# Performance work log

Measured on AMD Instinct MI355X. Metric: run time of the kernel, lower is better.

## Reference

```python
import jax, jax.numpy as jnp
import numpy as np

N_EXAMPLES = 10  # hardcoded repeat_interleave(10) in the source

def setup_inputs() -> dict:
    key = jax.random.key(0)
    k1, k2, k3, k4 = jax.random.split(key, 4)
    B, L, S, H = 8, 256, 512, 1024
    return {
        "output": jax.random.normal(k1, (B * N_EXAMPLES, L, H), dtype=jnp.float32),
        "context0": jax.random.normal(k2, (B * N_EXAMPLES, L, H), dtype=jnp.float32),
        "context1": jax.random.normal(k3, (B, S, H), dtype=jnp.float32),
        "mask": jnp.zeros((B * N_EXAMPLES, L), dtype=bool),
        "W_out": jax.random.normal(k4, (H, 3 * H), dtype=jnp.float32) * 0.02,
        "b_out": jnp.zeros((H,), dtype=jnp.float32),
    }

def reference(output, context0, context1, mask, W_out, b_out):
    # output, context0: [B*10, L, H]; context1: [B, S, H]
    # NOTE: in the torch source, `attn.data.masked_fill(mask, -inf)` is NOT
    # in-place and its result is discarded, so the mask has no effect on the
    # math. We reproduce that faithfully: `mask` is unused.
    del mask
    set_ctx = jnp.repeat(context1, N_EXAMPLES, axis=0)  # [B*10, S, H]
    # example-attention branch: bmm -> softmax -> bmm
    ex_attn = jax.nn.softmax(jnp.einsum('bld,bsd->bls', output, context0), axis=-1)  # [B*10, L, L]
    # set-attention branch: bmm -> softmax -> bmm
    set_attn = jax.nn.softmax(jnp.einsum('bld,bsd->bls', output, set_ctx), axis=-1)  # [B*10, L, S]
    ex_c = jnp.einsum('bls,bsd->bld', ex_attn, context0)   # [B*10, L, H]
    set_c = jnp.einsum('bls,bsd->bld', set_attn, set_ctx)  # [B*10, L, H]
    all_info = jnp.concatenate([output, ex_c, set_c], axis=-1)  # [B*10, L, 3H]
    out = jnp.tanh(jnp.einsum('blk,hk->blh', all_info, W_out) + b_out)  # [B*10, L, H]
    return (out, ex_attn, set_attn)
```

## Files before the change

### kernel.cpp

```cpp
#include <hip/hip_runtime.h>
#include <stdint.h>
#include <math.h>

typedef unsigned short u16;
typedef __attribute__((ext_vector_type(8))) short short8;
typedef __attribute__((ext_vector_type(4))) float floatx4;

__device__ __forceinline__ u16 f32_to_bf16(float f) {
    union { float f; uint32_t u; } v; v.f = f;
    uint32_t r = v.u + 0x7FFF + ((v.u >> 16) & 1);
    return (u16)(r >> 16);
}
__device__ __forceinline__ float bf16_to_f32(u16 h) {
    union { uint32_t u; float f; } v; v.u = ((uint32_t)h) << 16; return v.f;
}

__device__ __forceinline__ void gl_lds16(const u16* g, u16* l) {
    __builtin_amdgcn_global_load_lds(
        (const __attribute__((address_space(1))) void*)g,
        (__attribute__((address_space(3))) void*)l, 16, 0, 0);
}


__global__ void split_kernel(const float4* __restrict__ x, ushort4* __restrict__ hi,
                             ushort4* __restrict__ lo, long n4) {
    long i = (long)blockIdx.x * blockDim.x + threadIdx.x;
    if (i >= n4) return;
    float4 v = x[i];
    ushort4 h, l;
    h.x = f32_to_bf16(v.x); l.x = f32_to_bf16(v.x - bf16_to_f32(h.x));
    h.y = f32_to_bf16(v.y); l.y = f32_to_bf16(v.y - bf16_to_f32(h.y));
    h.z = f32_to_bf16(v.z); l.z = f32_to_bf16(v.z - bf16_to_f32(h.z));
    h.w = f32_to_bf16(v.w); l.w = f32_to_bf16(v.w - bf16_to_f32(h.w));
    hi[i] = h; lo[i] = l;
}

__global__ void conv_kernel(const float4* __restrict__ x, ushort4* __restrict__ hi, long n4) {
    long i = (long)blockIdx.x * blockDim.x + threadIdx.x;
    if (i >= n4) return;
    float4 v = x[i];
    ushort4 h;
    h.x = f32_to_bf16(v.x); h.y = f32_to_bf16(v.y);
    h.z = f32_to_bf16(v.z); h.w = f32_to_bf16(v.w);
    hi[i] = h;
}

__global__ void transpose_u16(const u16* __restrict__ src, u16* __restrict__ dst,
                              int R, int C) {
    __shared__ u16 tile[32][34];
    long base = (long)blockIdx.z * R * C;
    int c0 = blockIdx.x * 32, r0 = blockIdx.y * 32;
    #pragma unroll
    for (int i = threadIdx.y; i < 32; i += 8)
        tile[i][threadIdx.x] = src[base + (long)(r0 + i) * C + c0 + threadIdx.x];
    __syncthreads();
    #pragma unroll
    for (int i = threadIdx.y; i < 32; i += 8)
        dst[base + (long)(c0 + i) * R + r0 + threadIdx.x] = tile[threadIdx.x][i];
}

template <int VPT>
__global__ void softmax_rows(float* __restrict__ data, u16* __restrict__ outb) {
    int row = blockIdx.x * 4 + (threadIdx.x >> 6);
    int lane = threadIdx.x & 63;
    long base = (long)row * (VPT * 64) + lane;
    float v[VPT];
    #pragma unroll
    for (int i = 0; i < VPT; ++i) v[i] = data[base + i * 64];
    float m = v[0];
    #pragma unroll
    for (int i = 1; i < VPT; ++i) m = fmaxf(m, v[i]);
    #pragma unroll
    for (int off = 32; off > 0; off >>= 1) m = fmaxf(m, __shfl_xor(m, off, 64));
    float s = 0.f;
    #pragma unroll
    for (int i = 0; i < VPT; ++i) { v[i] = __expf(v[i] - m); s += v[i]; }
    #pragma unroll
    for (int off = 32; off > 0; off >>= 1) s += __shfl_xor(s, off, 64);
    float inv = 1.0f / s;
    #pragma unroll
    for (int i = 0; i < VPT; ++i) {
        float r = v[i] * inv;
        data[base + i * 64] = r;
        outb[base + i * 64] = f32_to_bf16(r);
    }
}

struct GemmP {
    const u16* A[3];
    const u16* B[3];
    const u16* B2[3];
    long strideAb, strideBb, strideB2b, strideCb, strideC2b;
    int bdiv, bdiv2, nseg, Kper, lda, ldb, ldb2, ldc, ldc2, mode;
    int gx, gy, nx1;
    float* Cf; float* Cf2; u16* Cb; const float* bias;
};

__global__ __launch_bounds__(256) void gemm_bt(GemmP p) {
    __shared__ u16 As[128 * 64];
    __shared__ u16 Bs[128 * 64];
    const int tid  = threadIdx.x;
    const int lane = tid & 63;
    const int wave = tid >> 6;
    const int quad = lane >> 4;
    const int l15  = lane & 15;
    const int wm = (wave & 1) * 64;
    const int wn = (wave >> 1) * 64;

    const int f  = blockIdx.x;
    const int Tx = gridDim.x >> 3;
    const int t  = (f & 7) * Tx + (f >> 3);
    const int n  = t % p.gx;
    const int r  = t / p.gx;
    const int m0 = (r % p.gy) * 128;
    const int bz = r / p.gy;

    const u16* Bsegs[3];
    int ldb, ldc, nn, bdv;
    long bstr, cstr;
    float* Cf;
    if (n < p.nx1) {
        Bsegs[0] = p.B[0]; Bsegs[1] = p.B[1]; Bsegs[2] = p.B[2];
        ldb = p.ldb; ldc = p.ldc; bstr = p.strideBb; cstr = p.strideCb;
        Cf = p.Cf; bdv = p.bdiv; nn = n;
    } else {
        Bsegs[0] = p.B2[0]; Bsegs[1] = p.B2[1]; Bsegs[2] = p.B2[2];
        ldb = p.ldb2; ldc = p.ldc2; bstr = p.strideB2b; cstr = p.strideC2b;
        Cf = p.Cf2; bdv = p.bdiv2; nn = n - p.nx1;
    }
    const int n0 = nn * 128;

    const int stg_r8 = tid >> 3;
    const int stg_c  = ((tid & 7) ^ (stg_r8 & 7)) * 8;
    const int xorl   = l15 & 7;

    floatx4 acc[4][4];
    #pragma unroll
    for (int i = 0; i < 4; ++i)
        #pragma unroll
        for (int j = 0; j < 4; ++j)
            acc[i][j] = (floatx4){0.f, 0.f, 0.f, 0.f};

    const long aoff = (long)bz * p.strideAb + (long)m0 * p.lda;
    const long boff = (long)(bz / bdv) * bstr + (long)n0 * ldb;

    for (int seg = 0; seg < p.nseg; ++seg) {
        const u16* Ag = p.A[seg] + aoff;
        const u16* Bg = Bsegs[seg] + boff;
        for (int k0 = 0; k0 < p.Kper; k0 += 64) {
            __syncthreads();
            #pragma unroll
            for (int i = 0; i < 4; ++i) {
                const int rr = i * 32 + stg_r8;
                gl_lds16(Ag + (long)rr * p.lda + k0 + stg_c, &As[(i * 256 + tid) * 8]);
            }
            #pragma unroll
            for (int i = 0; i < 4; ++i) {
                const int rr = i * 32 + stg_r8;
                gl_lds16(Bg + (long)rr * ldb + k0 + stg_c, &Bs[(i * 256 + tid) * 8]);
            }
            __syncthreads();
            #pragma unroll
            for (int kk = 0; kk < 2; ++kk) {
                const int cs = ((kk * 4 + quad) ^ xorl) * 8;
                short8 af[4], bfr[4];
                #pragma unroll
                for (int i = 0; i < 4; ++i)
                    af[i] = *(const short8*)&As[(wm + i * 16 + l15) * 64 + cs];
                #pragma unroll
                for (int i = 0; i < 4; ++i)
                    bfr[i] = *(const short8*)&Bs[(wn + i * 16 + l15) * 64 + cs];
                #pragma unroll
                for (int mi = 0; mi < 4; ++mi)
                    #pragma unroll
                    for (int ni = 0; ni < 4; ++ni)
                        acc[mi][ni] = __builtin_amdgcn_mfma_f32_16x16x32_bf16(
                            af[mi], bfr[ni], acc[mi][ni], 0, 0, 0);
            }
        }
    }

    const long coff = (long)bz * cstr;
    const int rb = m0 + wm + quad * 4;
    const int cbase = n0 + wn + l15;
    if (p.mode == 2) {
        #pragma unroll
        for (int ni = 0; ni < 4; ++ni) {
            const float bv = p.bias[cbase + ni * 16];
            #pragma unroll
            for (int mi = 0; mi < 4; ++mi)
                #pragma unroll
                for (int j = 0; j < 4; ++j)
                    Cf[coff + (long)(rb + mi * 16 + j) * ldc + cbase + ni * 16] =
                        tanhf(acc[mi][ni][j] + bv);
        }
    } else if (p.mode == 0) {
        #pragma unroll
        for (int ni = 0; ni < 4; ++ni)
            #pragma unroll
            for (int mi = 0; mi < 4; ++mi)
                #pragma unroll
                for (int j = 0; j < 4; ++j)
                    Cf[coff + (long)(rb + mi * 16 + j) * ldc + cbase + ni * 16] =
                        acc[mi][ni][j];
    } else {
        #pragma unroll
        for (int ni = 0; ni < 4; ++ni)
            #pragma unroll
            for (int mi = 0; mi < 4; ++mi)
                #pragma unroll
                for (int j = 0; j < 4; ++j)
                    p.Cb[coff + (long)(rb + mi * 16 + j) * ldc + cbase + ni * 16] =
                        f32_to_bf16(acc[mi][ni][j]);
    }
}

extern "C" void kernel_launch(void* const* d_in, const int* in_sizes, int n_in,
                              void* d_out, int out_size, void* d_ws, size_t ws_size,
                              hipStream_t stream) {
    const int BT = 80, L = 256, S = 512, H = 1024;
    const long NO    = (long)BT * L * H;
    const long NC1   = (long)8 * S * H;
    const long NW    = (long)H * 3 * H;
    const long NEXA  = (long)BT * L * L;
    const long NSETA = (long)BT * L * S;

    const float* X    = (const float*)d_in[0];
    const float* C0   = (const float*)d_in[1];
    const float* C1   = (const float*)d_in[2];
    const float* Wf   = (const float*)d_in[4];
    const float* bias = (const float*)d_in[5];

    float* out  = (float*)d_out;
    float* exa  = out + NO;
    float* seta = exa + NEXA;

    char* wsb = (char*)d_ws;
    size_t off = 0;
    auto alloc = [&](long nbytes) -> void* {
        void* p = (void*)(wsb + off);
        off += ((size_t)nbytes + 255) & ~(size_t)255;
        return p;
    };
    u16* Xhi  = (u16*)alloc(NO * 2);
    u16* Xlo  = (u16*)alloc(NO * 2);
    u16* C0hi = (u16*)alloc(NO * 2);
    u16* C0lo = (u16*)alloc(NO * 2);
    u16* C1hi = (u16*)alloc(NC1 * 2);
    u16* C1lo = (u16*)alloc(NC1 * 2);
    u16* Wb   = (u16*)alloc(NW * 2);
    u16* exab = (u16*)alloc(NEXA * 2);
    u16* setab= (u16*)alloc(NSETA * 2);
    u16* C0T = C0lo;
    u16* C1T = C1lo;
    u16* exc = Xlo;
    u16* setc = C0hi;

    split_kernel<<<(int)(NO / 4 / 256), 256, 0, stream>>>((const float4*)X, (ushort4*)Xhi, (ushort4*)Xlo, NO / 4);
    split_kernel<<<(int)(NO / 4 / 256), 256, 0, stream>>>((const float4*)C0, (ushort4*)C0hi, (ushort4*)C0lo, NO / 4);
    split_kernel<<<(int)(NC1 / 4 / 256), 256, 0, stream>>>((const float4*)C1, (ushort4*)C1hi, (ushort4*)C1lo, NC1 / 4);
    conv_kernel<<<(int)(NW / 4 / 256), 256, 0, stream>>>((const float4*)Wf, (ushort4*)Wb, NW / 4);

    {
        GemmP p{};
        p.A[0] = Xhi;  p.A[1] = Xlo;  p.A[2] = Xhi;
        p.B[0]  = C0hi; p.B[1]  = C0hi; p.B[2]  = C0lo;
        p.B2[0] = C1hi; p.B2[1] = C1hi; p.B2[2] = C1lo;
        p.strideAb = (long)L * H;
        p.strideBb = (long)L * H;  p.strideB2b = (long)S * H;
        p.strideCb = (long)L * L;  p.strideC2b = (long)L * S;
        p.bdiv = 1; p.bdiv2 = 10;
        p.nseg = 3; p.Kper = H; p.lda = H; p.ldb = H; p.ldb2 = H;
        p.ldc = L; p.ldc2 = S; p.mode = 0;
        p.gx = 6; p.gy = 2; p.nx1 = 2;
        p.Cf = exa; p.Cf2 = seta;
        gemm_bt<<<dim3(6 * 2 * BT, 1, 1), 256, 0, stream>>>(p);
    }
    softmax_rows<4><<<BT * L / 4, 256, 0, stream>>>(exa, exab);
    softmax_rows<8><<<BT * L / 4, 256, 0, stream>>>(seta, setab);

    transpose_u16<<<dim3(H / 32, L / 32, BT), dim3(32, 8), 0, stream>>>(C0hi, C0T, L, H);
    transpose_u16<<<dim3(H / 32, S / 32, 8), dim3(32, 8), 0, stream>>>(C1hi, C1T, S, H);

    {
        GemmP p{};
        p.A[0] = exab; p.B[0] = C0T;
        p.strideAb = (long)L * L; p.strideBb = (long)H * L; p.strideCb = (long)L * H;
        p.bdiv = 1; p.nseg = 1; p.Kper = L; p.lda = L; p.ldb = L; p.ldc = H; p.mode = 1;
        p.gx = 8; p.gy = 2; p.nx1 = 8;
        p.Cb = exc;
        gemm_bt<<<dim3(8 * 2 * BT, 1, 1), 256, 0, stream>>>(p);
    }
    {
        GemmP p{};
        p.A[0] = setab; p.B[0] = C1T;
        p.strideAb = (long)L * S; p.strideBb = (long)H * S; p.strideCb = (long)L * H;
        p.bdiv = 10; p.nseg = 1; p.Kper = S; p.lda = S; p.ldb = S; p.ldc = H; p.mode = 1;
        p.gx = 8; p.gy = 2; p.nx1 = 8;
        p.Cb = setc;
        gemm_bt<<<dim3(8 * 2 * BT, 1, 1), 256, 0, stream>>>(p);
    }
    {
        GemmP p{};
        p.A[0] = Xhi; p.A[1] = exc; p.A[2] = setc;
        p.B[0] = Wb;  p.B[1] = Wb + 1024; p.B[2] = Wb + 2048;
        p.strideAb = 0; p.strideBb = 0; p.strideCb = 0;
        p.bdiv = 1; p.nseg = 3; p.Kper = H; p.lda = H; p.ldb = 3 * H; p.ldc = H; p.mode = 2;
        p.gx = 8; p.gy = BT * L / 128; p.nx1 = 8;
        p.Cf = out; p.bias = bias;
        gemm_bt<<<dim3(8 * (BT * L / 128), 1, 1), 256, 0, stream>>>(p);
    }
}
```

Measured before the change: 756.3 us.

## Replace GEMM with 256x256-tile 8-wave kernel using double-buffered async LDS pipeline

Replaces the 128x128, 4-wave, single-buffered GEMM with a 256x256-tile, 8-wave kernel. It uses a flattened K loop across segments and double-buffered global-to-LDS loads issued between MFMA phases, with a new XOR swizzle, s_setprio and sched barriers. The aim is to raise data reuse per tile and hide global load latency behind MFMA work instead of syncing around every K step. The cost is 128KB of LDS and far fewer blocks (e.g. 240 for the attention GEMM), which may underfill the CUs and leaves tails for the small GEMMs.

```diff
diff --git a/kernel.cpp b/kernel.cpp
--- a/kernel.cpp
+++ b/kernel.cpp
@@ -91,28 +91,28 @@
     const u16* B[3];
     const u16* B2[3];
     long strideAb, strideBb, strideB2b, strideCb, strideC2b;
-    int bdiv, bdiv2, nseg, Kper, lda, ldb, ldb2, ldc, ldc2, mode;
+    int bdiv, bdiv2, kshift, kmask, nt, lda, ldb, ldb2, ldc, ldc2, mode;
     int gx, gy, nx1;
     float* Cf; float* Cf2; u16* Cb; const float* bias;
 };
 
-__global__ __launch_bounds__(256) void gemm_bt(GemmP p) {
-    __shared__ u16 As[128 * 64];
-    __shared__ u16 Bs[128 * 64];
+__global__ __launch_bounds__(512, 2) void gemm_bt8(GemmP p) {
+    __shared__ u16 As[32768];
+    __shared__ u16 Bs[32768];
     const int tid  = threadIdx.x;
     const int lane = tid & 63;
     const int wave = tid >> 6;
     const int quad = lane >> 4;
     const int l15  = lane & 15;
-    const int wm = (wave & 1) * 64;
-    const int wn = (wave >> 1) * 64;
+    const int wr   = wave >> 2;
+    const int wc   = wave & 3;
 
     const int f  = blockIdx.x;
     const int Tx = gridDim.x >> 3;
     const int t  = (f & 7) * Tx + (f >> 3);
     const int n  = t % p.gx;
     const int r  = t / p.gx;
-    const int m0 = (r % p.gy) * 128;
+    const int m0 = (r % p.gy) * 256;
     const int bz = r / p.gy;
 
     const u16* Bsegs[3];
@@ -128,89 +128,131 @@
         ldb = p.ldb2; ldc = p.ldc2; bstr = p.strideB2b; cstr = p.strideC2b;
         Cf = p.Cf2; bdv = p.bdiv2; nn = n - p.nx1;
     }
-    const int n0 = nn * 128;
-
-    const int stg_r8 = tid >> 3;
-    const int stg_c  = ((tid & 7) ^ (stg_r8 & 7)) * 8;
-    const int xorl   = l15 & 7;
-
-    floatx4 acc[4][4];
-    #pragma unroll
-    for (int i = 0; i < 4; ++i)
+    const int n0 = nn * 256;
+
+    const long aoff = (long)bz * p.strideAb + (long)m0 * p.lda;
+    const long boff = (long)(bz / bdv) * bstr + (long)n0 * ldb;
+
+    const int srow = tid >> 2;
+    const int sgc  = ((tid & 3) ^ ((srow >> 1) & 3)) * 8;
+
+    const int rA = wr * 128 + l15;
+    const u16* pA = As + rA * 32 + ((quad ^ ((rA >> 1) & 3)) * 8);
+    const int rB = wc * 64 + l15;
+    const u16* pB = Bs + rB * 32 + ((quad ^ ((rB >> 1) & 3)) * 8);
+
+    const int nt = p.nt;
+
+    auto stA = [&](int kt, int kk) {
+        if (kt < nt) {
+            const int seg = kt >> p.kshift;
+            const u16* g = p.A[seg] + aoff + (long)srow * p.lda
+                         + (((kt & p.kmask) << 6) + kk * 32 + sgc);
+            u16* d = &As[((((kt & 1) << 1) | kk) << 13) + tid * 8];
+            gl_lds16(g, d);
+            gl_lds16(g + (long)128 * p.lda, d + 4096);
+        }
+    };
+    auto stB = [&](int kt, int kk) {
+        if (kt < nt) {
+            const int seg = kt >> p.kshift;
+            const u16* g = Bsegs[seg] + boff + (long)srow * ldb
+                         + (((kt & p.kmask) << 6) + kk * 32 + sgc);
+            u16* d = &Bs[((((kt & 1) << 1) | kk) << 13) + tid * 8];
+            gl_lds16(g, d);
+            gl_lds16(g + (long)128 * ldb, d + 4096);
+        }
+    };
+
+    floatx4 acc[8][4];
+    #pragma unroll
+    for (int i = 0; i < 8; ++i)
         #pragma unroll
         for (int j = 0; j < 4; ++j)
             acc[i][j] = (floatx4){0.f, 0.f, 0.f, 0.f};
 
-    const long aoff = (long)bz * p.strideAb + (long)m0 * p.lda;
-    const long boff = (long)(bz / bdv) * bstr + (long)n0 * ldb;
-
-    for (int seg = 0; seg < p.nseg; ++seg) {
-        const u16* Ag = p.A[seg] + aoff;
-        const u16* Bg = Bsegs[seg] + boff;
-        for (int k0 = 0; k0 < p.Kper; k0 += 64) {
-            __syncthreads();
-            #pragma unroll
-            for (int i = 0; i < 4; ++i) {
-                const int rr = i * 32 + stg_r8;
-                gl_lds16(Ag + (long)rr * p.lda + k0 + stg_c, &As[(i * 256 + tid) * 8]);
-            }
-            #pragma unroll
-            for (int i = 0; i < 4; ++i) {
-                const int rr = i * 32 + stg_r8;
-                gl_lds16(Bg + (long)rr * ldb + k0 + stg_c, &Bs[(i * 256 + tid) * 8]);
-            }
-            __syncthreads();
-            #pragma unroll
-            for (int kk = 0; kk < 2; ++kk) {
-                const int cs = ((kk * 4 + quad) ^ xorl) * 8;
-                short8 af[4], bfr[4];
-                #pragma unroll
-                for (int i = 0; i < 4; ++i)
-                    af[i] = *(const short8*)&As[(wm + i * 16 + l15) * 64 + cs];
-                #pragma unroll
-                for (int i = 0; i < 4; ++i)
-                    bfr[i] = *(const short8*)&Bs[(wn + i * 16 + l15) * 64 + cs];
-                #pragma unroll
-                for (int mi = 0; mi < 4; ++mi)
-                    #pragma unroll
-                    for (int ni = 0; ni < 4; ++ni)
-                        acc[mi][ni] = __builtin_amdgcn_mfma_f32_16x16x32_bf16(
-                            af[mi], bfr[ni], acc[mi][ni], 0, 0, 0);
-            }
+    stA(0, 0); stB(0, 0); stA(0, 1); stB(0, 1); stA(1, 0); stB(1, 0);
+    asm volatile("s_waitcnt vmcnt(4)" ::: "memory");
+    __builtin_amdgcn_s_barrier();
+
+    short8 af[4], bf[4];
+
+#define QPHASE(SO, MH, LOADB, STAGE)                                        \
+    {                                                                       \
+        _Pragma("unroll")                                                   \
+        for (int mi = 0; mi < 4; ++mi)                                      \
+            af[mi] = *(const short8*)(pA + (SO) + (MH) * 2048 + mi * 512);  \
+        if (LOADB) {                                                        \
+            _Pragma("unroll")                                               \
+            for (int ni = 0; ni < 4; ++ni)                                  \
+                bf[ni] = *(const short8*)(pB + (SO) + ni * 512);            \
+        }                                                                   \
+        STAGE;                                                              \
+        __builtin_amdgcn_s_barrier();                                       \
+        asm volatile("s_waitcnt lgkmcnt(0)" ::: "memory");                  \
+        __builtin_amdgcn_sched_barrier(0);                                  \
+        __builtin_amdgcn_s_setprio(1);                                      \
+        _Pragma("unroll")                                                   \
+        for (int mi = 0; mi < 4; ++mi)                                      \
+            _Pragma("unroll")                                               \
+            for (int ni = 0; ni < 4; ++ni)                                  \
+                acc[(MH) * 4 + mi][ni] =                                    \
+                    __builtin_amdgcn_mfma_f32_16x16x32_bf16(                \
+                        af[mi], bf[ni], acc[(MH) * 4 + mi][ni], 0, 0, 0);   \
+        __builtin_amdgcn_s_setprio(0);                                      \
+        __builtin_amdgcn_sched_barrier(0);                                  \
+    }
+
+    for (int kt = 0; kt < nt; ++kt) {
+        const int so0 = (kt & 1) << 14;
+        const int so1 = so0 + 8192;
+        QPHASE(so0, 0, true,  stA(kt + 1, 1));
+        __builtin_amdgcn_s_barrier();
+        QPHASE(so0, 1, false, stB(kt + 1, 1));
+        __builtin_amdgcn_s_barrier();
+        QPHASE(so1, 0, true,  stA(kt + 2, 0));
+        __builtin_amdgcn_s_barrier();
+        QPHASE(so1, 1, false, stB(kt + 2, 0));
+        if (kt + 2 < nt) {
+            asm volatile("s_waitcnt vmcnt(4)" ::: "memory");
+        } else {
+            asm volatile("s_waitcnt vmcnt(0)" ::: "memory");
         }
-    }
+        __builtin_amdgcn_s_barrier();
+    }
+#undef QPHASE
 
     const long coff = (long)bz * cstr;
-    const int rb = m0 + wm + quad * 4;
-    const int cbase = n0 + wn + l15;
+    const int rb = m0 + wr * 128 + quad * 4;
+    const int cb = n0 + wc * 64 + l15;
     if (p.mode == 2) {
         #pragma unroll
         for (int ni = 0; ni < 4; ++ni) {
-            const float bv = p.bias[cbase + ni * 16];
+            const float bv = p.bias[cb + ni * 16];
             #pragma unroll
-            for (int mi = 0; mi < 4; ++mi)
+            for (int mi = 0; mi < 8; ++mi)
                 #pragma unroll
                 for (int j = 0; j < 4; ++j)
-                    Cf[coff + (long)(rb + mi * 16 + j) * ldc + cbase + ni * 16] =
+                    Cf[coff + (long)(rb + mi * 16 + j) * ldc + cb + ni * 16] =
                         tanhf(acc[mi][ni][j] + bv);
         }
     } else if (p.mode == 0) {
         #pragma unroll
         for (int ni = 0; ni < 4; ++ni)
             #pragma unroll
-            for (int mi = 0; mi < 4; ++mi)
+            for (int mi = 0; mi < 8; ++mi)
                 #pragma unroll
                 for (int j = 0; j < 4; ++j)
-                    Cf[coff + (long)(rb + mi * 16 + j) * ldc + cbase + ni * 16] =
+                    Cf[coff + (long)(rb + mi * 16 + j) * ldc + cb + ni * 16] =
                         acc[mi][ni][j];
     } else {
         #pragma unroll
         for (int ni = 0; ni < 4; ++ni)
             #pragma unroll
-            for (int mi = 0; mi < 4; ++mi)
+            for (int mi = 0; mi < 8; ++mi)
                 #pragma unroll
                 for (int j = 0; j < 4; ++j)
-                    p.Cb[coff + (long)(rb + mi * 16 + j) * ldc + cbase + ni * 16] =
+                    p.Cb[coff + (long)(rb + mi * 16 + j) * ldc + cb + ni * 16] =
                         f32_to_bf16(acc[mi][ni][j]);
     }
 }
@@ -270,11 +312,12 @@
         p.strideBb = (long)L * H;  p.strideB2b = (long)S * H;
         p.strideCb = (long)L * L;  p.strideC2b = (long)L * S;
         p.bdiv = 1; p.bdiv2 = 10;
-        p.nseg = 3; p.Kper = H; p.lda = H; p.ldb = H; p.ldb2 = H;
+        p.kshift = 4; p.kmask = 15; p.nt = 48;
+        p.lda = H; p.ldb = H; p.ldb2 = H;
         p.ldc = L; p.ldc2 = S; p.mode = 0;
-        p.gx = 6; p.gy = 2; p.nx1 = 2;
+        p.gx = 3; p.gy = 1; p.nx1 = 1;
         p.Cf = exa; p.Cf2 = seta;
-        gemm_bt<<<dim3(6 * 2 * BT, 1, 1), 256, 0, stream>>>(p);
+        gemm_bt8<<<dim3(3 * 1 * BT, 1, 1), 512, 0, stream>>>(p);
     }
     softmax_rows<4><<<BT * L / 4, 256, 0, stream>>>(exa, exab);
     softmax_rows<8><<<BT * L / 4, 256, 0, stream>>>(seta, setab);
@@ -286,28 +329,31 @@
         GemmP p{};
         p.A[0] = exab; p.B[0] = C0T;
         p.strideAb = (long)L * L; p.strideBb = (long)H * L; p.strideCb = (long)L * H;
-        p.bdiv = 1; p.nseg = 1; p.Kper = L; p.lda = L; p.ldb = L; p.ldc = H; p.mode = 1;
-        p.gx = 8; p.gy = 2; p.nx1 = 8;
+        p.bdiv = 1; p.kshift = 2; p.kmask = 3; p.nt = 4;
+        p.lda = L; p.ldb = L; p.ldc = H; p.mode = 1;
+        p.gx = 4; p.gy = 1; p.nx1 = 4;
         p.Cb = exc;
-        gemm_bt<<<dim3(8 * 2 * BT, 1, 1), 256, 0, stream>>>(p);
+        gemm_bt8<<<dim3(4 * 1 * BT, 1, 1), 512, 0, stream>>>(p);
     }
     {
         GemmP p{};
         p.A[0] = setab; p.B[0] = C1T;
         p.strideAb = (long)L * S; p.strideBb = (long)H * S; p.strideCb = (long)L * H;
-        p.bdiv = 10; p.nseg = 1; p.Kper = S; p.lda = S; p.ldb = S; p.ldc = H; p.mode = 1;
-        p.gx = 8; p.gy = 2; p.nx1 = 8;
+        p.bdiv = 10; p.kshift = 3; p.kmask = 7; p.nt = 8;
+        p.lda = S; p.ldb = S; p.ldc = H; p.mode = 1;
+        p.gx = 4; p.gy = 1; p.nx1 = 4;
         p.Cb = setc;
-        gemm_bt<<<dim3(8 * 2 * BT, 1, 1), 256, 0, stream>>>(p);
+        gemm_bt8<<<dim3(4 * 1 * BT, 1, 1), 512, 0, stream>>>(p);
     }
     {
         GemmP p{};
         p.A[0] = Xhi; p.A[1] = exc; p.A[2] = setc;
         p.B[0] = Wb;  p.B[1] = Wb + 1024; p.B[2] = Wb + 2048;
         p.strideAb = 0; p.strideBb = 0; p.strideCb = 0;
-        p.bdiv = 1; p.nseg = 3; p.Kper = H; p.lda = H; p.ldb = 3 * H; p.ldc = H; p.mode = 2;
-        p.gx = 8; p.gy = BT * L / 128; p.nx1 = 8;
+        p.bdiv = 1; p.kshift = 4; p.kmask = 15; p.nt = 48;
+        p.lda = H; p.ldb = 3 * H; p.ldc = H; p.mode = 2;
+        p.gx = 4; p.gy = BT * L / 256; p.nx1 = 4;
         p.Cf = out; p.bias = bias;
-        gemm_bt<<<dim3(8 * (BT * L / 128), 1, 1), 256, 0, stream>>>(p);
-    }
-}
+        gemm_bt8<<<dim3(4 * (BT * L / 256), 1, 1), 512, 0, stream>>>(p);
+    }
+}
```

Result: slower. 775.0 us (+2.5%).
